# Kernel tuning notes

Hardware: AMD Instinct MI355X
Metric: run time of the kernel (lower is better)

## Reference

```python
import jax, jax.numpy as jnp
import numpy as np

EPS = 1e-8
SMOOTH = 9.0
N_IMAGE, N_REGIONS, N_CAP, MAX_WORDS = 64, 36, 64, 40
EMBED, SIM_DIM = 1024, 256


def l2norm(x, axis=-1):
    n = jnp.sqrt(jnp.sum(x * x, axis=axis, keepdims=True)) + EPS
    return x / n


def setup_inputs() -> dict:
    key = jax.random.key(0)
    k1, k2, k3, k4 = jax.random.split(key, 4)
    img_emb = jax.random.normal(k1, (N_IMAGE, N_REGIONS, EMBED), dtype=jnp.float32)
    cap_emb = jax.random.normal(k2, (N_CAP, MAX_WORDS, EMBED), dtype=jnp.float32)
    cap_lens = jax.random.randint(k3, (N_CAP,), 10, MAX_WORDS + 1)
    # zero out padded words so the batched formulation matches the per-caption loop
    mask = (jnp.arange(MAX_WORDS)[None, :] < cap_lens[:, None]).astype(jnp.float32)
    cap_emb = cap_emb * mask[:, :, None]
    adjs = jnp.zeros((N_CAP, MAX_WORDS, MAX_WORDS), dtype=jnp.int32)
    depends = jnp.zeros((N_CAP, MAX_WORDS, MAX_WORDS), dtype=jnp.int32)
    r = np.sqrt(6.0) / np.sqrt(EMBED + SIM_DIM)
    W = jax.random.uniform(k4, (EMBED, SIM_DIM), minval=-r, maxval=r, dtype=jnp.float32)
    b = jnp.zeros((SIM_DIM,), dtype=jnp.float32)
    return {"img_emb": img_emb, "cap_emb": cap_emb, "cap_lens": cap_lens,
            "adjs": adjs, "depends": depends, "W": W, "b": b}


def reference(img_emb, cap_emb, cap_lens, adjs, depends, W, b):
    C, L, D = cap_emb.shape
    mask = (jnp.arange(L)[None, :] < cap_lens[:, None]).astype(cap_emb.dtype)  # (C, L)
    cap = cap_emb * mask[:, :, None]
    # attn: (C, I, R, L) = context . query^T for every (caption, image) pair
    attn = jnp.einsum('ird,cld->cirl', img_emb, cap)
    attn = jax.nn.leaky_relu(attn, negative_slope=0.1)
    # l2norm over the word dim (padded words contribute exactly 0)
    attn = attn / (jnp.sqrt(jnp.sum(attn * attn, axis=3, keepdims=True)) + EPS)
    # softmax over regions after transpose + smooth scaling: (C, I, L, R)
    attn = jax.nn.softmax(jnp.swapaxes(attn, 2, 3) * SMOOTH, axis=3)
    wc = jnp.einsum('cilr,ird->cild', attn, img_emb)  # (C, I, L, D)
    wc = l2norm(wc, axis=-1)
    sim = jnp.square(wc - cap[:, None, :, :])
    out = l2norm(jax.nn.relu(sim @ W + b), axis=-1)
    # zero padded-word rows (the original returns only :n_word slices)
    out = out * mask[:, None, :, None]
    return out  # (C, I, L, SIM_DIM)
```

## Files before the change

### kernel.cpp

```cpp
#include <hip/hip_runtime.h>

#define C_N 64
#define I_N 64
#define R_N 36
#define L_N 40
#define D_N 1024
#define S_N 256

#define P_LD 72

#define OFF_CAP 2359296
#define OFF_WT  4980736
#define OFF_IMT 5242880
#define OFF_SLK 8388608
#define OFF_SIM 8388672
#define M_ALL   (C_N * I_N * L_N)
#define CH_STRIDE ((size_t)M_ALL * 32)
#define OFF_G   (OFF_SIM + 32 * CH_STRIDE)


typedef float f4 __attribute__((ext_vector_type(4)));
typedef short s16x8 __attribute__((ext_vector_type(8)));
typedef short s16x4 __attribute__((ext_vector_type(4)));

__device__ __forceinline__ unsigned short f2bs(float f) {
    union { float f; unsigned u; } v; v.f = f;
    unsigned r = v.u + 0x7FFFu + ((v.u >> 16) & 1u);
    return (unsigned short)(r >> 16);
}
__device__ __forceinline__ float bs2f(unsigned short s) {
    union { unsigned u; float f; } v; v.u = ((unsigned)s) << 16;
    return v.f;
}
__device__ __forceinline__ void async16(const unsigned short* g, unsigned short* l) {
    __builtin_amdgcn_global_load_lds(
        (const __attribute__((address_space(1))) unsigned int*)g,
        (__attribute__((address_space(3))) unsigned int*)l, 16, 0, 0);
}

__global__ void k_convert(const float* __restrict__ img, const float* __restrict__ cap,
                          const float* __restrict__ W, unsigned short* __restrict__ ws) {
    int t = blockIdx.x * 256 + threadIdx.x;
    if (t < I_N * R_N * D_N) ws[t] = f2bs(img[t]);
    if (t < C_N * L_N * D_N) ws[OFF_CAP + t] = f2bs(cap[t]);
    if (t < D_N * S_N) {
        int d = t >> 8, s = t & 255;
        int ch = d >> 5, wi = d & 31;
        int md = wi >> 4, r = wi & 15, q = r >> 2, j = r & 3;
        int ep = q * 8 + md * 4 + j;
        ws[OFF_WT + ((ch * 256 + s) * 32) + ep] = f2bs(W[t]);
    }
    if (t < 64) ws[OFF_SLK + t] = 0;
}

__global__ __launch_bounds__(256)
void k_imt(const float* __restrict__ img, unsigned short* __restrict__ imt) {
    __shared__ unsigned short t[64][50];
    const int i = blockIdx.y, d0 = blockIdx.x * 64;
    const int tid = threadIdx.x;
    #pragma unroll
    for (int it = 0; it < 9; ++it) {
        int e = it * 256 + tid;
        int r = e >> 6, dc = e & 63;
        t[dc][r] = f2bs(img[((size_t)i * R_N + r) * D_N + d0 + dc]);
    }
    #pragma unroll
    for (int it = 0; it < 3; ++it) {
        int e = it * 256 + tid;
        t[e & 63][36 + (e >> 6)] = 0;
    }
    __syncthreads();
    #pragma unroll
    for (int it = 0; it < 6; ++it) {
        int e = it * 256 + tid;
        int dc = e / 24, wd = e - dc * 24;
        unsigned v = (unsigned)t[dc][2 * wd] | ((unsigned)t[dc][2 * wd + 1] << 16);
        ((unsigned*)imt)[(size_t)(i * D_N + d0 + dc) * 24 + wd] = v;
    }
}

__global__ __launch_bounds__(64)
void k_gram(const unsigned short* __restrict__ img_b, unsigned short* __restrict__ g) {
    const int i = blockIdx.x;
    const int lane = threadIdx.x;
    const int q = lane >> 4, ln16 = lane & 15;
    const unsigned short* ai = img_b + i * (R_N * D_N);
    unsigned short* gi = g + i * (48 * 64);
    for (int e = lane; e < 48 * 8; e += 64) {
        int r = e >> 3, wd = e & 7;
        ((unsigned*)(gi + r * 64 + 48))[wd] = 0;
    }
    f4 c[3][3] = {};
    #pragma unroll 4
    for (int ks = 0; ks < 32; ++ks) {
        const int kb = ks * 32 + q * 8;
        s16x8 af[3];
        af[0] = *(const s16x8*)(ai + ln16 * D_N + kb);
        af[1] = *(const s16x8*)(ai + (16 + ln16) * D_N + kb);
        af[2] = (ln16 < 4) ? *(const s16x8*)(ai + (32 + ln16) * D_N + kb) : (s16x8)0;
        #pragma unroll
        for (int mt = 0; mt < 3; ++mt)
            #pragma unroll
            for (int nt = 0; nt < 3; ++nt)
                c[mt][nt] = __builtin_amdgcn_mfma_f32_16x16x32_bf16(af[mt], af[nt], c[mt][nt], 0, 0, 0);
    }
    #pragma unroll
    for (int mt = 0; mt < 3; ++mt)
        #pragma unroll
        for (int nt = 0; nt < 3; ++nt)
            #pragma unroll
            for (int j = 0; j < 4; ++j)
                gi[(mt * 16 + q * 4 + j) * 64 + nt * 16 + ln16] = f2bs(c[mt][nt][j]);
}

__global__ __launch_bounds__(512, 4)
void k_pre(const unsigned short* __restrict__ img_b,
           const unsigned short* __restrict__ cap_b,
           const unsigned short* __restrict__ img_t,
           const unsigned short* __restrict__ gram,
           unsigned short* __restrict__ simg) {
    __shared__ __align__(16) unsigned short s_p[8][48 * P_LD];

    const int n = blockIdx.y * 8 + blockIdx.x;
    const int x = n & 7, m = n >> 3;
    const int i   = ((x & 3) << 4) | (m >> 2);
    const int oct = ((x >> 2) << 2) | (m & 3);
    const int wave = threadIdx.x >> 6, lane = threadIdx.x & 63;
    const int c = oct * 8 + wave;
    const int pair = c * I_N + i;
    const int q = lane >> 4, ln16 = lane & 15;

    const unsigned short* ai = img_b + i * (R_N * D_N);
    const unsigned short* bc = cap_b + c * (L_N * D_N);
    const unsigned short* imtc = img_t + (size_t)i * D_N * 48;
    unsigned short* sp = &s_p[wave][0];

    for (int k = lane; k < 48 * P_LD / 2; k += 64) ((unsigned*)sp)[k] = 0;

    f4 acc[3][3] = {};
    #pragma unroll 4
    for (int ks = 0; ks < 32; ++ks) {
        const int kb = ks * 32 + q * 8;
        s16x8 af[3], bf[3];
        af[0] = *(const s16x8*)(ai + ln16 * D_N + kb);
        af[1] = *(const s16x8*)(ai + (16 + ln16) * D_N + kb);
        af[2] = (ln16 < 4) ? *(const s16x8*)(ai + (32 + ln16) * D_N + kb) : (s16x8)0;
        bf[0] = *(const s16x8*)(bc + ln16 * D_N + kb);
        bf[1] = *(const s16x8*)(bc + (16 + ln16) * D_N + kb);
        bf[2] = (ln16 < 8) ? *(const s16x8*)(bc + (32 + ln16) * D_N + kb) : (s16x8)0;
        #pragma unroll
        for (int mt = 0; mt < 3; ++mt)
            #pragma unroll
            for (int nt = 0; nt < 3; ++nt)
                acc[mt][nt] = __builtin_amdgcn_mfma_f32_16x16x32_bf16(af[mt], bf[nt], acc[mt][nt], 0, 0, 0);
    }

    #pragma unroll
    for (int mt = 0; mt < 3; ++mt)
        #pragma unroll
        for (int nt = 0; nt < 3; ++nt)
            #pragma unroll
            for (int j = 0; j < 4; ++j) {
                float v = acc[mt][nt][j];
                acc[mt][nt][j] = (v > 0.f) ? v : 0.1f * v;
            }
    #pragma unroll
    for (int mt = 0; mt < 3; ++mt)
        #pragma unroll
        for (int j = 0; j < 4; ++j) {
            float ss = 0.f;
            #pragma unroll
            for (int nt = 0; nt < 3; ++nt) ss += acc[mt][nt][j] * acc[mt][nt][j];
            #pragma unroll
            for (int o = 1; o < 16; o <<= 1) ss += __shfl_xor(ss, o, 64);
            float inv = 1.f / (sqrtf(ss) + 1e-8f);
            #pragma unroll
            for (int nt = 0; nt < 3; ++nt) acc[mt][nt][j] *= inv;
        }
    #pragma unroll
    for (int nt = 0; nt < 3; ++nt) {
        const int l = nt * 16 + ln16;
        float mx = -1e30f;
        #pragma unroll
        for (int mt = 0; mt < 3; ++mt)
            #pragma unroll
            for (int j = 0; j < 4; ++j) {
                int r = mt * 16 + q * 4 + j;
                if (r < R_N) mx = fmaxf(mx, 9.f * acc[mt][nt][j]);
            }
        mx = fmaxf(mx, __shfl_xor(mx, 16, 64));
        mx = fmaxf(mx, __shfl_xor(mx, 32, 64));
        float sum = 0.f;
        #pragma unroll
        for (int mt = 0; mt < 3; ++mt)
            #pragma unroll
            for (int j = 0; j < 4; ++j) {
                int r = mt * 16 + q * 4 + j;
                float e = (r < R_N) ? __expf(9.f * acc[mt][nt][j] - mx) : 0.f;
                acc[mt][nt][j] = e;
                sum += e;
            }
        sum += __shfl_xor(sum, 16, 64);
        sum += __shfl_xor(sum, 32, 64);
        float inv = 1.f / sum;
        #pragma unroll
        for (int mt = 0; mt < 3; ++mt)
            #pragma unroll
            for (int j = 0; j < 4; ++j) {
                int r = mt * 16 + q * 4 + j;
                if (r < R_N && l < L_N) sp[l * P_LD + r] = f2bs(acc[mt][nt][j] * inv);
            }
    }

    s16x8 paf[3][2];
    #pragma unroll
    for (int nl = 0; nl < 3; ++nl)
        #pragma unroll
        for (int ks = 0; ks < 2; ++ks)
            paf[nl][ks] = *(const s16x8*)(sp + (nl * 16 + ln16) * P_LD + ks * 32 + q * 8);

    const unsigned short* gi = gram + i * (48 * 64);
    f4 T[3][3] = {};
    #pragma unroll
    for (int ks = 0; ks < 2; ++ks) {
        const int kb = ks * 32 + q * 8;
        s16x8 ga[3];
        #pragma unroll
        for (int mt = 0; mt < 3; ++mt)
            ga[mt] = *(const s16x8*)(gi + (mt * 16 + ln16) * 64 + kb);
        #pragma unroll
        for (int mt = 0; mt < 3; ++mt)
            #pragma unroll
            for (int nl = 0; nl < 3; ++nl)
                T[mt][nl] = __builtin_amdgcn_mfma_f32_16x16x32_bf16(ga[mt], paf[nl][ks], T[mt][nl], 0, 0, 0);
    }
    float inv2[3];
    #pragma unroll
    for (int nl = 0; nl < 3; ++nl) {
        const int l = nl * 16 + ln16;
        float rsl = 0.f;
        #pragma unroll
        for (int mt = 0; mt < 3; ++mt) {
            const s16x4 pv = *(const s16x4*)(sp + l * P_LD + mt * 16 + q * 4);
            #pragma unroll
            for (int j = 0; j < 4; ++j)
                rsl += bs2f((unsigned short)pv[j]) * T[mt][nl][j];
        }
        rsl += __shfl_xor(rsl, 16, 64);
        rsl += __shfl_xor(rsl, 32, 64);
        inv2[nl] = 1.f / (sqrtf(rsl) + 1e-8f);
    }

    #pragma unroll 2
    for (int ch = 0; ch < 32; ++ch) {
        f4 a2[2][3] = {};
        #pragma unroll
        for (int ks = 0; ks < 2; ++ks) {
            const int kb = ks * 32 + q * 8;
            #pragma unroll
            for (int md = 0; md < 2; ++md) {
                const int drow = ch * 32 + md * 16 + ln16;
                s16x8 afr = *(const s16x8*)(imtc + drow * 48 + kb);
                #pragma unroll
                for (int nl = 0; nl < 3; ++nl)
                    a2[md][nl] = __builtin_amdgcn_mfma_f32_16x16x32_bf16(afr, paf[nl][ks], a2[md][nl], 0, 0, 0);
            }
        }
        const size_t chbase = (size_t)ch * CH_STRIDE + (size_t)pair * L_N * 32;
        #pragma unroll
        for (int nl = 0; nl < 3; ++nl) {
            const int l = nl * 16 + ln16;
            if (l < L_N) {
                const float iv = inv2[nl];
                s16x8 ov;
                #pragma unroll
                for (int md = 0; md < 2; ++md) {
                    const int db = ch * 32 + md * 16 + q * 4;
                    const s16x4 cv = *(const s16x4*)(bc + l * D_N + db);
                    #pragma unroll
                    for (int j = 0; j < 4; ++j) {
                        float dv = a2[md][nl][j] * iv - bs2f((unsigned short)cv[j]);
                        ov[md * 4 + j] = (short)f2bs(dv * dv);
                    }
                }
                __builtin_nontemporal_store(ov,
                    (s16x8*)(simg + chbase + (size_t)l * 32 + q * 8));
            }
        }
    }
}

__global__ __launch_bounds__(512, 4)
void k_gemm3(const unsigned short* __restrict__ simt,
             const unsigned short* __restrict__ wtt,
             const int* __restrict__ cap_lens,
             const float* __restrict__ bias,
             float* __restrict__ out) {
    __shared__ __align__(16) unsigned short sA[2][128 * 32];
    __shared__ __align__(16) unsigned short sB[2][256 * 32];
    __shared__ float s_sum[128];

    const int tid = threadIdx.x;
    const int w = tid >> 6, lane = tid & 63;
    const int ln16 = lane & 15, q = lane >> 4;
    const int wm = (w >> 2) * 64, wn = (w & 3) * 64;
    const int m0 = blockIdx.x * 128;
    const int srow = tid >> 2;
    const int swz = ((tid & 3) ^ ((srow >> 1) & 3)) << 3;
    const unsigned short* gA  = simt + ((size_t)(m0 + srow)) * 32 + swz;
    const unsigned short* gB0 = wtt + (size_t)srow * 32 + swz;
    const unsigned short* gB1 = wtt + (size_t)(128 + srow) * 32 + swz;
    unsigned short* const lA = (unsigned short*)sA + tid * 8;
    unsigned short* const lB = (unsigned short*)sB + tid * 8;

    if (tid < 128) s_sum[tid] = 0.f;

    async16(gA + (size_t)31 * CH_STRIDE, lA);
    async16(gB0 + 31 * 8192, lB);
    async16(gB1 + 31 * 8192, lB + 4096);

    f4 acc[4][4] = {};
    #pragma unroll 1
    for (int t = 0; t < 31; ++t) {
        const int nb = (t + 1) & 1;
        const int pch = 30 - t;
        async16(gA + (size_t)pch * CH_STRIDE, lA + nb * 4096);
        async16(gB0 + pch * 8192, lB + nb * 8192);
        async16(gB1 + pch * 8192, lB + nb * 8192 + 4096);
        asm volatile("s_waitcnt vmcnt(3)" ::: "memory");
        __builtin_amdgcn_s_barrier();
        __builtin_amdgcn_sched_barrier(0);
        const unsigned short* cA = (const unsigned short*)sA + (t & 1) * 4096;
        const unsigned short* cB = (const unsigned short*)sB + (t & 1) * 8192;
        s16x8 af[4], bf[4];
        #pragma unroll
        for (int mt = 0; mt < 4; ++mt) {
            int row = wm + mt * 16 + ln16;
            af[mt] = *(const s16x8*)(cA + row * 32 + ((q ^ ((row >> 1) & 3)) << 3));
        }
        #pragma unroll
        for (int nt = 0; nt < 4; ++nt) {
            int row = wn + nt * 16 + ln16;
            bf[nt] = *(const s16x8*)(cB + row * 32 + ((q ^ ((row >> 1) & 3)) << 3));
        }
        #pragma unroll
        for (int mt = 0; mt < 4; ++mt)
            #pragma unroll
            for (int nt = 0; nt < 4; ++nt)
                acc[mt][nt] = __builtin_amdgcn_mfma_f32_16x16x32_bf16(af[mt], bf[nt], acc[mt][nt], 0, 0, 0);
        __builtin_amdgcn_s_barrier();
    }
    asm volatile("s_waitcnt vmcnt(0)" ::: "memory");
    __builtin_amdgcn_s_barrier();
    __builtin_amdgcn_sched_barrier(0);
    {
        const unsigned short* cA = (const unsigned short*)sA + 4096;
        const unsigned short* cB = (const unsigned short*)sB + 8192;
        s16x8 af[4], bf[4];
        #pragma unroll
        for (int mt = 0; mt < 4; ++mt) {
            int row = wm + mt * 16 + ln16;
            af[mt] = *(const s16x8*)(cA + row * 32 + ((q ^ ((row >> 1) & 3)) << 3));
        }
        #pragma unroll
        for (int nt = 0; nt < 4; ++nt) {
            int row = wn + nt * 16 + ln16;
            bf[nt] = *(const s16x8*)(cB + row * 32 + ((q ^ ((row >> 1) & 3)) << 3));
        }
        #pragma unroll
        for (int mt = 0; mt < 4; ++mt)
            #pragma unroll
            for (int nt = 0; nt < 4; ++nt)
                acc[mt][nt] = __builtin_amdgcn_mfma_f32_16x16x32_bf16(af[mt], bf[nt], acc[mt][nt], 0, 0, 0);
    }

    float bv[4];
    #pragma unroll
    for (int nt = 0; nt < 4; ++nt) bv[nt] = bias[wn + nt * 16 + ln16];
    #pragma unroll
    for (int mt = 0; mt < 4; ++mt)
        #pragma unroll
        for (int j = 0; j < 4; ++j) {
            float s = 0.f;
            #pragma unroll
            for (int nt = 0; nt < 4; ++nt) {
                float v = acc[mt][nt][j] + bv[nt];
                v = fmaxf(v, 0.f);
                acc[mt][nt][j] = v;
                s += v * v;
            }
            #pragma unroll
            for (int o = 1; o < 16; o <<= 1) s += __shfl_xor(s, o, 64);
            if (ln16 == 0) atomicAdd(&s_sum[wm + mt * 16 + q * 4 + j], s);
        }
    __syncthreads();
    if (tid < 128) {
        int grow = m0 + tid;
        int c = grow / (I_N * L_N);
        int l = grow % L_N;
        float inv = 1.f / (sqrtf(s_sum[tid]) + 1e-8f);
        s_sum[tid] = (l < cap_lens[c]) ? inv : 0.f;
    }
    __syncthreads();
    #pragma unroll
    for (int mt = 0; mt < 4; ++mt)
        #pragma unroll
        for (int j = 0; j < 4; ++j) {
            const int rt = wm + mt * 16 + q * 4 + j;
            const float sc = s_sum[rt];
            #pragma unroll
            for (int nt = 0; nt < 4; ++nt)
                __builtin_nontemporal_store(acc[mt][nt][j] * sc,
                    &out[(size_t)(m0 + rt) * S_N + wn + nt * 16 + ln16]);
        }
}

extern "C" void kernel_launch(void* const* d_in, const int* in_sizes, int n_in,
                              void* d_out, int out_size, void* d_ws, size_t ws_size,
                              hipStream_t stream) {
    const float* img  = (const float*)d_in[0];
    const float* cap  = (const float*)d_in[1];
    const int*   lens = (const int*)d_in[2];
    const float* W    = (const float*)d_in[5];
    const float* bias = (const float*)d_in[6];
    float* out = (float*)d_out;
    unsigned short* ws = (unsigned short*)d_ws;

    k_convert<<<10240, 256, 0, stream>>>(img, cap, W, ws);
    dim3 gridT(16, I_N);
    k_imt<<<gridT, 256, 0, stream>>>(img, ws + OFF_IMT);
    k_gram<<<I_N, 64, 0, stream>>>(ws, ws + OFF_G);

    dim3 gridP(8, I_N);
    k_pre<<<gridP, 512, 0, stream>>>(ws, ws + OFF_CAP, ws + OFF_IMT, ws + OFF_G,
                                     ws + OFF_SIM);

    k_gemm3<<<M_ALL / 128, 512, 0, stream>>>(ws + OFF_SIM, ws + OFF_WT, lens, bias, out);
}
```

Measured before the change: 508.7 us.

## Compact valid caption words and skip padded-word work across kernels

Adds a prefix scan over caption lengths so k_pre writes only valid word rows into a compacted sim buffer. k_gemm3 then processes only the valid rows, exits early for blocks past the valid count, and scatters its results back through a binary search over the scan. k_pre also skips MFMA tiles and softmax for word tiles beyond the caption length. Padded output rows are zeroed by a separate kernel. This cuts GEMM and elementwise work for padded words but adds two small kernels and per-row index arithmetic in the epilogue.

```diff
diff --git a/kernel.cpp b/kernel.cpp
--- a/kernel.cpp
+++ b/kernel.cpp
@@ -17,7 +17,7 @@
 #define M_ALL   (C_N * I_N * L_N)
 #define CH_STRIDE ((size_t)M_ALL * 32)
 #define OFF_G   (OFF_SIM + 32 * CH_STRIDE)
-
+#define OFF_P   (OFF_G + I_N * 48 * 64)
 
 typedef float f4 __attribute__((ext_vector_type(4)));
 typedef short s16x8 __attribute__((ext_vector_type(8)));
@@ -53,6 +53,26 @@
     if (t < 64) ws[OFF_SLK + t] = 0;
 }
 
+__global__ void k_scan(const int* __restrict__ lens, int* __restrict__ P) {
+    if (threadIdx.x == 0) {
+        int a = 0;
+        for (int c = 0; c < C_N; ++c) { P[c] = a; a += lens[c]; }
+        P[C_N] = a;
+    }
+}
+
+__global__ __launch_bounds__(256)
+void k_zero(const int* __restrict__ lens, float* __restrict__ out) {
+    int idx = blockIdx.x * 256 + threadIdx.x;
+    int row = idx >> 6, sq = (idx & 63) << 2;
+    int c = row / (I_N * L_N);
+    int l = row % L_N;
+    if (l >= lens[c]) {
+        f4 z = {};
+        __builtin_nontemporal_store(z, (f4*)(out + (size_t)row * S_N + sq));
+    }
+}
+
 __global__ __launch_bounds__(256)
 void k_imt(const float* __restrict__ img, unsigned short* __restrict__ imt) {
     __shared__ unsigned short t[64][50];
@@ -118,6 +138,8 @@
            const unsigned short* __restrict__ cap_b,
            const unsigned short* __restrict__ img_t,
            const unsigned short* __restrict__ gram,
+           const int* __restrict__ lens,
+           const int* __restrict__ P,
            unsigned short* __restrict__ simg) {
     __shared__ __align__(16) unsigned short s_p[8][48 * P_LD];
 
@@ -127,8 +149,11 @@
     const int oct = ((x >> 2) << 2) | (m & 3);
     const int wave = threadIdx.x >> 6, lane = threadIdx.x & 63;
     const int c = oct * 8 + wave;
-    const int pair = c * I_N + i;
     const int q = lane >> 4, ln16 = lane & 15;
+
+    const int len = lens[c];
+    const int NL = (len > 32) ? 3 : (len > 16 ? 2 : 1);
+    const int rowbase = P[c] * 64 + i * len;
 
     const unsigned short* ai = img_b + i * (R_N * D_N);
     const unsigned short* bc = cap_b + c * (L_N * D_N);
@@ -146,13 +171,14 @@
         af[1] = *(const s16x8*)(ai + (16 + ln16) * D_N + kb);
         af[2] = (ln16 < 4) ? *(const s16x8*)(ai + (32 + ln16) * D_N + kb) : (s16x8)0;
         bf[0] = *(const s16x8*)(bc + ln16 * D_N + kb);
-        bf[1] = *(const s16x8*)(bc + (16 + ln16) * D_N + kb);
-        bf[2] = (ln16 < 8) ? *(const s16x8*)(bc + (32 + ln16) * D_N + kb) : (s16x8)0;
+        bf[1] = (NL > 1) ? *(const s16x8*)(bc + (16 + ln16) * D_N + kb) : (s16x8)0;
+        bf[2] = (NL > 2 && ln16 < 8) ? *(const s16x8*)(bc + (32 + ln16) * D_N + kb) : (s16x8)0;
         #pragma unroll
         for (int mt = 0; mt < 3; ++mt)
             #pragma unroll
             for (int nt = 0; nt < 3; ++nt)
-                acc[mt][nt] = __builtin_amdgcn_mfma_f32_16x16x32_bf16(af[mt], bf[nt], acc[mt][nt], 0, 0, 0);
+                if (nt < NL)
+                    acc[mt][nt] = __builtin_amdgcn_mfma_f32_16x16x32_bf16(af[mt], bf[nt], acc[mt][nt], 0, 0, 0);
     }
 
     #pragma unroll
@@ -179,37 +205,39 @@
         }
     #pragma unroll
     for (int nt = 0; nt < 3; ++nt) {
-        const int l = nt * 16 + ln16;
-        float mx = -1e30f;
-        #pragma unroll
-        for (int mt = 0; mt < 3; ++mt)
-            #pragma unroll
-            for (int j = 0; j < 4; ++j) {
-                int r = mt * 16 + q * 4 + j;
-                if (r < R_N) mx = fmaxf(mx, 9.f * acc[mt][nt][j]);
-            }
-        mx = fmaxf(mx, __shfl_xor(mx, 16, 64));
-        mx = fmaxf(mx, __shfl_xor(mx, 32, 64));
-        float sum = 0.f;
-        #pragma unroll
-        for (int mt = 0; mt < 3; ++mt)
-            #pragma unroll
-            for (int j = 0; j < 4; ++j) {
-                int r = mt * 16 + q * 4 + j;
-                float e = (r < R_N) ? __expf(9.f * acc[mt][nt][j] - mx) : 0.f;
-                acc[mt][nt][j] = e;
-                sum += e;
-            }
-        sum += __shfl_xor(sum, 16, 64);
-        sum += __shfl_xor(sum, 32, 64);
-        float inv = 1.f / sum;
-        #pragma unroll
-        for (int mt = 0; mt < 3; ++mt)
-            #pragma unroll
-            for (int j = 0; j < 4; ++j) {
-                int r = mt * 16 + q * 4 + j;
-                if (r < R_N && l < L_N) sp[l * P_LD + r] = f2bs(acc[mt][nt][j] * inv);
-            }
+        if (nt < NL) {
+            const int l = nt * 16 + ln16;
+            float mx = -1e30f;
+            #pragma unroll
+            for (int mt = 0; mt < 3; ++mt)
+                #pragma unroll
+                for (int j = 0; j < 4; ++j) {
+                    int r = mt * 16 + q * 4 + j;
+                    if (r < R_N) mx = fmaxf(mx, 9.f * acc[mt][nt][j]);
+                }
+            mx = fmaxf(mx, __shfl_xor(mx, 16, 64));
+            mx = fmaxf(mx, __shfl_xor(mx, 32, 64));
+            float sum = 0.f;
+            #pragma unroll
+            for (int mt = 0; mt < 3; ++mt)
+                #pragma unroll
+                for (int j = 0; j < 4; ++j) {
+                    int r = mt * 16 + q * 4 + j;
+                    float e = (r < R_N) ? __expf(9.f * acc[mt][nt][j] - mx) : 0.f;
+                    acc[mt][nt][j] = e;
+                    sum += e;
+                }
+            sum += __shfl_xor(sum, 16, 64);
+            sum += __shfl_xor(sum, 32, 64);
+            float inv = 1.f / sum;
+            #pragma unroll
+            for (int mt = 0; mt < 3; ++mt)
+                #pragma unroll
+                for (int j = 0; j < 4; ++j) {
+                    int r = mt * 16 + q * 4 + j;
+                    if (r < R_N && l < L_N) sp[l * P_LD + r] = f2bs(acc[mt][nt][j] * inv);
+                }
+        }
     }
 
     s16x8 paf[3][2];
@@ -232,23 +260,26 @@
         for (int mt = 0; mt < 3; ++mt)
             #pragma unroll
             for (int nl = 0; nl < 3; ++nl)
-                T[mt][nl] = __builtin_amdgcn_mfma_f32_16x16x32_bf16(ga[mt], paf[nl][ks], T[mt][nl], 0, 0, 0);
-    }
-    float inv2[3];
+                if (nl < NL)
+                    T[mt][nl] = __builtin_amdgcn_mfma_f32_16x16x32_bf16(ga[mt], paf[nl][ks], T[mt][nl], 0, 0, 0);
+    }
+    float inv2[3] = {0.f, 0.f, 0.f};
     #pragma unroll
     for (int nl = 0; nl < 3; ++nl) {
-        const int l = nl * 16 + ln16;
-        float rsl = 0.f;
-        #pragma unroll
-        for (int mt = 0; mt < 3; ++mt) {
-            const s16x4 pv = *(const s16x4*)(sp + l * P_LD + mt * 16 + q * 4);
-            #pragma unroll
-            for (int j = 0; j < 4; ++j)
-                rsl += bs2f((unsigned short)pv[j]) * T[mt][nl][j];
-        }
-        rsl += __shfl_xor(rsl, 16, 64);
-        rsl += __shfl_xor(rsl, 32, 64);
-        inv2[nl] = 1.f / (sqrtf(rsl) + 1e-8f);
+        if (nl < NL) {
+            const int l = nl * 16 + ln16;
+            float rsl = 0.f;
+            #pragma unroll
+            for (int mt = 0; mt < 3; ++mt) {
+                const s16x4 pv = *(const s16x4*)(sp + l * P_LD + mt * 16 + q * 4);
+                #pragma unroll
+                for (int j = 0; j < 4; ++j)
+                    rsl += bs2f((unsigned short)pv[j]) * T[mt][nl][j];
+            }
+            rsl += __shfl_xor(rsl, 16, 64);
+            rsl += __shfl_xor(rsl, 32, 64);
+            inv2[nl] = 1.f / (sqrtf(rsl) + 1e-8f);
+        }
     }
 
     #pragma unroll 2
@@ -263,28 +294,31 @@
                 s16x8 afr = *(const s16x8*)(imtc + drow * 48 + kb);
                 #pragma unroll
                 for (int nl = 0; nl < 3; ++nl)
-                    a2[md][nl] = __builtin_amdgcn_mfma_f32_16x16x32_bf16(afr, paf[nl][ks], a2[md][nl], 0, 0, 0);
-            }
-        }
-        const size_t chbase = (size_t)ch * CH_STRIDE + (size_t)pair * L_N * 32;
+                    if (nl < NL)
+                        a2[md][nl] = __builtin_amdgcn_mfma_f32_16x16x32_bf16(afr, paf[nl][ks], a2[md][nl], 0, 0, 0);
+            }
+        }
+        const size_t chbase = (size_t)ch * CH_STRIDE + (size_t)rowbase * 32;
         #pragma unroll
         for (int nl = 0; nl < 3; ++nl) {
-            const int l = nl * 16 + ln16;
-            if (l < L_N) {
-                const float iv = inv2[nl];
-                s16x8 ov;
-                #pragma unroll
-                for (int md = 0; md < 2; ++md) {
-                    const int db = ch * 32 + md * 16 + q * 4;
-                    const s16x4 cv = *(const s16x4*)(bc + l * D_N + db);
+            if (nl < NL) {
+                const int l = nl * 16 + ln16;
+                if (l < len) {
+                    const float iv = inv2[nl];
+                    s16x8 ov;
                     #pragma unroll
-                    for (int j = 0; j < 4; ++j) {
-                        float dv = a2[md][nl][j] * iv - bs2f((unsigned short)cv[j]);
-                        ov[md * 4 + j] = (short)f2bs(dv * dv);
+                    for (int md = 0; md < 2; ++md) {
+                        const int db = ch * 32 + md * 16 + q * 4;
+                        const s16x4 cv = *(const s16x4*)(bc + l * D_N + db);
+                        #pragma unroll
+                        for (int j = 0; j < 4; ++j) {
+                            float dv = a2[md][nl][j] * iv - bs2f((unsigned short)cv[j]);
+                            ov[md * 4 + j] = (short)f2bs(dv * dv);
+                        }
                     }
+                    __builtin_nontemporal_store(ov,
+                        (s16x8*)(simg + chbase + (size_t)l * 32 + q * 8));
                 }
-                __builtin_nontemporal_store(ov,
-                    (s16x8*)(simg + chbase + (size_t)l * 32 + q * 8));
             }
         }
     }
@@ -293,18 +327,21 @@
 __global__ __launch_bounds__(512, 4)
 void k_gemm3(const unsigned short* __restrict__ simt,
              const unsigned short* __restrict__ wtt,
-             const int* __restrict__ cap_lens,
+             const int* __restrict__ P,
              const float* __restrict__ bias,
              float* __restrict__ out) {
     __shared__ __align__(16) unsigned short sA[2][128 * 32];
     __shared__ __align__(16) unsigned short sB[2][256 * 32];
     __shared__ float s_sum[128];
 
+    const int m0 = blockIdx.x * 128;
+    const int Mv = P[C_N] * 64;
+    if (m0 >= Mv) return;
+
     const int tid = threadIdx.x;
     const int w = tid >> 6, lane = tid & 63;
     const int ln16 = lane & 15, q = lane >> 4;
     const int wm = (w >> 2) * 64, wn = (w & 3) * 64;
-    const int m0 = blockIdx.x * 128;
     const int srow = tid >> 2;
     const int swz = ((tid & 3) ^ ((srow >> 1) & 3)) << 3;
     const unsigned short* gA  = simt + ((size_t)(m0 + srow)) * 32 + swz;
@@ -396,10 +433,7 @@
     __syncthreads();
     if (tid < 128) {
         int grow = m0 + tid;
-        int c = grow / (I_N * L_N);
-        int l = grow % L_N;
-        float inv = 1.f / (sqrtf(s_sum[tid]) + 1e-8f);
-        s_sum[tid] = (l < cap_lens[c]) ? inv : 0.f;
+        s_sum[tid] = (grow < Mv) ? 1.f / (sqrtf(s_sum[tid]) + 1e-8f) : 0.f;
     }
     __syncthreads();
     #pragma unroll
@@ -407,11 +441,24 @@
         #pragma unroll
         for (int j = 0; j < 4; ++j) {
             const int rt = wm + mt * 16 + q * 4 + j;
-            const float sc = s_sum[rt];
-            #pragma unroll
-            for (int nt = 0; nt < 4; ++nt)
-                __builtin_nontemporal_store(acc[mt][nt][j] * sc,
-                    &out[(size_t)(m0 + rt) * S_N + wn + nt * 16 + ln16]);
+            const int grow = m0 + rt;
+            if (grow < Mv) {
+                int lo = 0, hi = C_N;
+                while (hi - lo > 1) {
+                    int mid = (lo + hi) >> 1;
+                    if (P[mid] * 64 <= grow) lo = mid; else hi = mid;
+                }
+                const int lenc = P[lo + 1] - P[lo];
+                const int rem = grow - P[lo] * 64;
+                const int ii = rem / lenc;
+                const int ll = rem - ii * lenc;
+                const float sc = s_sum[rt];
+                float* op = out + (size_t)((lo * I_N + ii) * L_N + ll) * S_N + wn;
+                #pragma unroll
+                for (int nt = 0; nt < 4; ++nt)
+                    __builtin_nontemporal_store(acc[mt][nt][j] * sc,
+                        op + nt * 16 + ln16);
+            }
         }
 }
 
@@ -425,15 +472,18 @@
     const float* bias = (const float*)d_in[6];
     float* out = (float*)d_out;
     unsigned short* ws = (unsigned short*)d_ws;
+    int* P = (int*)(ws + OFF_P);
 
     k_convert<<<10240, 256, 0, stream>>>(img, cap, W, ws);
+    k_scan<<<1, 64, 0, stream>>>(lens, P);
+    k_zero<<<M_ALL / 4, 256, 0, stream>>>(lens, out);
     dim3 gridT(16, I_N);
     k_imt<<<gridT, 256, 0, stream>>>(img, ws + OFF_IMT);
     k_gram<<<I_N, 64, 0, stream>>>(ws, ws + OFF_G);
 
     dim3 gridP(8, I_N);
     k_pre<<<gridP, 512, 0, stream>>>(ws, ws + OFF_CAP, ws + OFF_IMT, ws + OFF_G,
-                                     ws + OFF_SIM);
-
-    k_gemm3<<<M_ALL / 128, 512, 0, stream>>>(ws + OFF_SIM, ws + OFF_WT, lens, bias, out);
-}
+                                     lens, P, ws + OFF_SIM);
+
+    k_gemm3<<<M_ALL / 128, 512, 0, stream>>>(ws + OFF_SIM, ws + OFF_WT, P, bias, out);
+}
```

Result: faster. 477.0 us (-6.2%).
